# Kernel tuning notes

Measured on AMD Instinct MI355X. Metric: run time of the kernel, lower is better.

The kernel has to match this reference:

```python
import jax, jax.numpy as jnp
import numpy as np

N_Q, N_X, N_Z = 512, 256, 256
N = N_Q + N_X + N_Z  # 1024 nodes per graph
H = 128
B = 128
EPS = 1e-5


def _bn(x, g, b):
    # BatchNorm1d in training mode: biased stats over all but last axis
    ax = tuple(range(x.ndim - 1))
    m = x.mean(ax)
    v = x.var(ax)
    return (x - m) * jax.lax.rsqrt(v + EPS) * g + b


def _node_feats():
    # buffer 'single_nodes': one-hot [qubit, x-check, z-check]
    f = jnp.zeros((N, 3), jnp.float32)
    f = f.at[:N_Q, 0].set(1.0)
    f = f.at[N_Q:N_Q + N_X, 1].set(1.0)
    f = f.at[N_Q + N_X:, 2].set(1.0)
    return f


def setup_inputs() -> dict:
    key = jax.random.key(0)
    ks = jax.random.split(key, 16)

    def lin(k, i, o):
        return (jax.random.normal(k, (i, o), jnp.float32) / np.sqrt(i)).astype(jnp.float32)

    return {
        "adj": jax.random.randint(ks[0], (B, N, N), 0, 2, dtype=jnp.int32),
        "w0a": lin(ks[1], 3, H), "b0a": jnp.zeros((H,), jnp.float32),
        "w0b": lin(ks[2], H, H), "b0b": jnp.zeros((H,), jnp.float32),
        "w1a": lin(ks[3], H, H), "b1a": jnp.zeros((H,), jnp.float32),
        "w1b": lin(ks[4], H, H), "b1b": jnp.zeros((H,), jnp.float32),
        "w2a": lin(ks[5], H, H), "b2a": jnp.zeros((H,), jnp.float32),
        "w2b": lin(ks[6], H, H), "b2b": jnp.zeros((H,), jnp.float32),
        "bn_in_g": jnp.ones((3,), jnp.float32), "bn_in_b": jnp.zeros((3,), jnp.float32),
        "bn0_g": jnp.ones((H,), jnp.float32), "bn0_b": jnp.zeros((H,), jnp.float32),
        "bn1_g": jnp.ones((H,), jnp.float32), "bn1_b": jnp.zeros((H,), jnp.float32),
        "bn2_g": jnp.ones((H,), jnp.float32), "bn2_b": jnp.zeros((H,), jnp.float32),
        "ln_g": jnp.ones((H,), jnp.float32), "ln_b": jnp.zeros((H,), jnp.float32),
        "fc1_w": lin(ks[7], H, 256), "fc1_b": jnp.zeros((256,), jnp.float32),
        "fcbn1_g": jnp.ones((256,), jnp.float32), "fcbn1_b": jnp.zeros((256,), jnp.float32),
        "fc2_w": lin(ks[8], 256, 512), "fc2_b": jnp.zeros((512,), jnp.float32),
        "fcbn2_g": jnp.ones((512,), jnp.float32), "fcbn2_b": jnp.zeros((512,), jnp.float32),
        "fc3_w": lin(ks[9], 512, 1), "fc3_b": jnp.zeros((1,), jnp.float32),
    }


def reference(adj, w0a, b0a, w0b, b0b, w1a, b1a, w1b, b1b, w2a, b2a, w2b, b2b,
              bn_in_g, bn_in_b, bn0_g, bn0_b, bn1_g, bn1_b, bn2_g, bn2_b,
              ln_g, ln_b, fc1_w, fc1_b, fcbn1_g, fcbn1_b, fc2_w, fc2_b,
              fcbn2_g, fcbn2_b, fc3_w, fc3_b):
    leaky = lambda z: jax.nn.leaky_relu(z, 0.1)
    Af = adj.astype(jnp.float32)                       # [B,N,N]
    x = jnp.broadcast_to(_node_feats(), (adj.shape[0], N, 3))
    x = _bn(x, bn_in_g, bn_in_b)                       # input BatchNorm1d(3)
    h = x

    mlps = [(w0a, b0a, w0b, b0b, jax.nn.relu, bn0_g, bn0_b),
            (w1a, b1a, w1b, b1b, leaky, bn1_g, bn1_b),
            (w2a, b2a, w2b, b2b, leaky, bn2_g, bn2_b)]
    for i, (wa, ba, wb, bb, act, g, b) in enumerate(mlps):
        # GINConv (eps=0): aggregate = h_i + sum_{j: edge j->i} h_j = h + A^T h
        agg = h + jnp.einsum('bji,bjd->bid', Af, h)
        m = act(agg @ wa + ba) @ wb + bb               # GIN MLP
        m = _bn(m, g, b)
        h = jax.nn.relu(m + (h if i > 0 else 0.0))

    pooled = h.mean(axis=1)                            # global_mean_pool -> [B,H]
    mu = pooled.mean(-1, keepdims=True)
    var = pooled.var(-1, keepdims=True)
    out = (pooled - mu) * jax.lax.rsqrt(var + EPS) * ln_g + ln_b  # LayerNorm

    z = leaky(_bn(out @ fc1_w + fc1_b, fcbn1_g, fcbn1_b))
    z = leaky(_bn(z @ fc2_w + fc2_b, fcbn2_g, fcbn2_b))
    return z @ fc3_w + fc3_b                           # [B,1]
```

## Files before the change

### kernel.cpp

```cpp
#include <hip/hip_runtime.h>
#include <hip/hip_bf16.h>

typedef float f32x4 __attribute__((ext_vector_type(4)));
typedef _Float16 half8 __attribute__((ext_vector_type(8)));
typedef _Float16 half4 __attribute__((ext_vector_type(4)));

__device__ __forceinline__ unsigned short f2h(float f) {
  return __builtin_bit_cast(unsigned short, (_Float16)f);
}
__device__ __forceinline__ float h2f(unsigned short u) {
  return (float)__builtin_bit_cast(_Float16, u);
}
__device__ __forceinline__ unsigned expand2(unsigned b2) {
  return (b2 & 1u) * 0x3C00u + ((b2 >> 1) & 1u) * 0x3C000000u;
}
__device__ __forceinline__ half8 expand8(unsigned v) {
  uint4 u;
  u.x = expand2(v);
  u.y = expand2(v >> 2);
  u.z = expand2(v >> 4);
  u.w = expand2(v >> 6);
  return __builtin_bit_cast(half8, u);
}

__global__ __launch_bounds__(256) void k_pack(const int* __restrict__ adj,
    unsigned* __restrict__ Abits, float* __restrict__ cnt,
    const float* __restrict__ w0b, const float* __restrict__ w1a,
    const float* __restrict__ w1b, const float* __restrict__ w2a,
    const float* __restrict__ w2b, unsigned short* __restrict__ wT) {
  __shared__ int tile[64 * 129];
  __shared__ unsigned bitT[128 * 33];
  __shared__ float cred[256 * 3];
  int blk = blockIdx.x;
  if (blk >= 1024) {
    int wb = blk - 1024;
    if (threadIdx.x < 128) {
      int mat = wb >> 7, k = wb & 127, dd = threadIdx.x;
      const float* src = (mat == 0) ? w0b : (mat == 1) ? w1a : (mat == 2) ? w1b
                        : (mat == 3) ? w2a : w2b;
      wT[mat * 16384 + dd * 128 + k] = f2h(src[k * 128 + dd]);
    }
    return;
  }
  int b = blk >> 3, i0 = (blk & 7) << 7;
  int t = threadIdx.x;
  int il = t & 127, js = t >> 7;
  int c0 = 0, c1 = 0, c2 = 0;
  for (int jt = 0; jt < 16; ++jt) {
    int jbase = jt << 6;
    __syncthreads();
    for (int p = 0; p < 8; ++p) {
      int f = p * 256 + t;
      int row = f >> 5, i4 = (f & 31) << 2;
      *reinterpret_cast<int4*>(&tile[row * 129 + i4]) =
        *reinterpret_cast<const int4*>(&adj[((size_t)b << 20) + ((size_t)(jbase + row) << 10) + i0 + i4]);
    }
    __syncthreads();
    unsigned wbits = 0;
    int csum = 0;
    for (int r = 0; r < 32; ++r) {
      int jl = js * 32 + r;
      int a = tile[jl * 129 + il] & 1;
      csum += a;
      wbits |= (unsigned)a << r;
    }
    bitT[il * 33 + jt * 2 + js] = wbits;
    if (jt < 8) c0 += csum; else if (jt < 12) c1 += csum; else c2 += csum;
  }
  cred[t * 3 + 0] = (float)c0;
  cred[t * 3 + 1] = (float)c1;
  cred[t * 3 + 2] = (float)c2;
  __syncthreads();
  if (t < 128) {
    for (int c = 0; c < 3; ++c)
      cnt[(((size_t)b << 10) + i0 + t) * 4 + c] = cred[t * 3 + c] + cred[(t + 128) * 3 + c];
  }
  unsigned* dst = Abits + ((size_t)b << 15) + ((size_t)i0 << 5);
  for (int q = 0; q < 16; ++q) {
    int f = t + 256 * q;
    dst[f] = bitT[(f >> 5) * 33 + (f & 31)];
  }
}

__global__ __launch_bounds__(256) void k_layer(const unsigned* __restrict__ Abits,
    const unsigned short* __restrict__ h_t,
    const unsigned short* __restrict__ waT, const float* __restrict__ ba,
    const unsigned short* __restrict__ wbT, const float* __restrict__ bb,
    unsigned short* __restrict__ m_out, float* __restrict__ ps, float* __restrict__ pq) {
  __shared__ __align__(16) unsigned short smem[18432];
  unsigned short* tb0 = smem;
  unsigned short* tb1 = smem + 9216;
  unsigned short* tz = smem;
  int d = blockIdx.x;
  int b = (d & 7) + ((d >> 6) << 3);
  int i0 = ((d >> 3) & 7) << 7;
  int t = threadIdx.x;
  int w = t >> 6, lane = t & 63;
  int wr = (w >> 1) * 64, wc = (w & 1) * 64;
  int lr = lane & 15, lk8 = (lane >> 4) * 8;
  const unsigned* Ab = Abits + ((size_t)b << 15);

  f32x4 acc[4][4] = {};
  {
    for (int q = 0; q < 4; ++q) {
      int c = t * 4 + q;
      int r = c >> 3, off = (c & 7) << 3;
      *reinterpret_cast<uint4*>(&tb0[r * 72 + off]) =
        *reinterpret_cast<const uint4*>(&h_t[(((size_t)b << 7) + r) * 1024 + off]);
    }
  }
  __syncthreads();
  for (int jt = 0; jt < 16; ++jt) {
    unsigned short* cur = (jt & 1) ? tb1 : tb0;
    unsigned short* nxt = (jt & 1) ? tb0 : tb1;
    if (jt < 15) {
      for (int q = 0; q < 4; ++q) {
        int c = t * 4 + q;
        int r = c >> 3, off = (c & 7) << 3;
        *reinterpret_cast<uint4*>(&nxt[r * 72 + off]) =
          *reinterpret_cast<const uint4*>(&h_t[(((size_t)b << 7) + r) * 1024 + ((jt + 1) << 6) + off]);
      }
    }
    uint2 w01[4];
#pragma unroll
    for (int x = 0; x < 4; ++x)
      w01[x] = *reinterpret_cast<const uint2*>(&Ab[(i0 + wr + x * 16 + lr) * 32 + jt * 2]);
#pragma unroll
    for (int ks = 0; ks < 2; ++ks) {
      half8 bfr[4];
#pragma unroll
      for (int x = 0; x < 4; ++x)
        bfr[x] = *reinterpret_cast<const half8*>(&cur[(wc + x * 16 + lr) * 72 + ks * 32 + lk8]);
      half8 af[4];
#pragma unroll
      for (int x = 0; x < 4; ++x) {
        unsigned wk = ks ? w01[x].y : w01[x].x;
        af[x] = expand8(wk >> lk8);
      }
#pragma unroll
      for (int x = 0; x < 4; ++x)
#pragma unroll
        for (int y = 0; y < 4; ++y)
          acc[x][y] = __builtin_amdgcn_mfma_f32_16x16x32_f16(af[x], bfr[y], acc[x][y], 0, 0, 0);
    }
    __syncthreads();
  }
  for (int x = 0; x < 4; ++x)
    for (int y = 0; y < 4; ++y) {
      int col = wc + y * 16 + lr;
      int row0 = wr + x * 16 + ((lane >> 4) << 2);
      uint2 rbits = *reinterpret_cast<const uint2*>(
          &h_t[((size_t)(b * 128 + col)) * 1024 + i0 + row0]);
      half4 rh = __builtin_bit_cast(half4, rbits);
      for (int q = 0; q < 4; ++q)
        tz[(row0 + q) * 136 + col] = f2h(acc[x][y][q] + (float)rh[q]);
    }
  __syncthreads();
  f32x4 acc2[4][4] = {};
#pragma unroll
  for (int kt = 0; kt < 2; ++kt)
#pragma unroll
    for (int ks = 0; ks < 2; ++ks) {
      int k0 = kt * 64 + ks * 32 + lk8;
      half8 af[4], bw[4];
#pragma unroll
      for (int x = 0; x < 4; ++x)
        af[x] = *reinterpret_cast<const half8*>(&tz[(wr + x * 16 + lr) * 136 + k0]);
#pragma unroll
      for (int x = 0; x < 4; ++x)
        bw[x] = *reinterpret_cast<const half8*>(&waT[(wc + x * 16 + lr) * 128 + k0]);
#pragma unroll
      for (int x = 0; x < 4; ++x)
#pragma unroll
        for (int y = 0; y < 4; ++y)
          acc2[x][y] = __builtin_amdgcn_mfma_f32_16x16x32_f16(af[x], bw[y], acc2[x][y], 0, 0, 0);
    }
  __syncthreads();
  for (int x = 0; x < 4; ++x)
    for (int y = 0; y < 4; ++y)
      for (int q = 0; q < 4; ++q) {
        int row = wr + x * 16 + ((lane >> 4) << 2) + q;
        int col = wc + y * 16 + lr;
        float vv = acc2[x][y][q] + ba[col];
        vv = vv > 0.f ? vv : 0.1f * vv;
        tz[row * 136 + col] = f2h(vv);
      }
  __syncthreads();
  f32x4 acc3[4][4] = {};
#pragma unroll
  for (int kt = 0; kt < 2; ++kt)
#pragma unroll
    for (int ks = 0; ks < 2; ++ks) {
      int k0 = kt * 64 + ks * 32 + lk8;
      half8 af[4], bw[4];
#pragma unroll
      for (int x = 0; x < 4; ++x)
        af[x] = *reinterpret_cast<const half8*>(&tz[(wr + x * 16 + lr) * 136 + k0]);
#pragma unroll
      for (int x = 0; x < 4; ++x)
        bw[x] = *reinterpret_cast<const half8*>(&wbT[(wc + x * 16 + lr) * 128 + k0]);
#pragma unroll
      for (int x = 0; x < 4; ++x)
#pragma unroll
        for (int y = 0; y < 4; ++y)
          acc3[x][y] = __builtin_amdgcn_mfma_f32_16x16x32_f16(af[x], bw[y], acc3[x][y], 0, 0, 0);
    }
  float s[4] = {}, q2[4] = {};
  for (int x = 0; x < 4; ++x)
    for (int y = 0; y < 4; ++y)
      for (int q = 0; q < 4; ++q) {
        int row = wr + x * 16 + ((lane >> 4) << 2) + q;
        int col = wc + y * 16 + lr;
        float vv = acc3[x][y][q] + bb[col];
        m_out[(((size_t)b << 10) + i0 + row) * 128 + col] = f2h(vv);
        s[y] += vv; q2[y] += vv * vv;
      }
  __syncthreads();
  float* fs = (float*)smem;
  float* fq = fs + 1024;
  int slot = (w >> 1) * 4 + (lane >> 4);
  for (int y = 0; y < 4; ++y) {
    int col = wc + y * 16 + lr;
    fs[col * 8 + slot] = s[y];
    fq[col * 8 + slot] = q2[y];
  }
  __syncthreads();
  if (t < 128) {
    float S = 0, Q = 0;
    for (int k = 0; k < 8; ++k) { S += fs[t * 8 + k]; Q += fq[t * 8 + k]; }
    ps[d * 128 + t] = S;
    pq[d * 128 + t] = Q;
  }
}

__global__ __launch_bounds__(256) void k_layer0(const float* __restrict__ cnt,
    const float* __restrict__ w0a, const float* __restrict__ b0a,
    const float* __restrict__ g3, const float* __restrict__ bb3,
    const unsigned short* __restrict__ wbT, const float* __restrict__ bb,
    unsigned short* __restrict__ m_out, float* __restrict__ ps, float* __restrict__ pq) {
  __shared__ __align__(16) unsigned short smem[17408];
  unsigned short* tz = smem;
  int blk = blockIdx.x;
  int b = blk >> 3, i0 = (blk & 7) << 7;
  int t = threadIdx.x;
  int w = t >> 6, lane = t & 63;
  int wr = (w >> 1) * 64, wc = (w & 1) * 64;
  int lr = lane & 15, lk8 = (lane >> 4) * 8;

  const float mean3[3] = {0.5f, 0.25f, 0.25f};
  const float var3[3] = {0.25f, 0.1875f, 0.1875f};
  float v[3][3];
  for (int c = 0; c < 3; ++c) {
    float rs = rsqrtf(var3[c] + 1e-5f) * g3[c];
    for (int tt = 0; tt < 3; ++tt)
      v[tt][c] = ((tt == c ? 1.f : 0.f) - mean3[c]) * rs + bb3[c];
  }
  int rr = t >> 1, hf = t & 1;
  int i = i0 + rr;
  int ty = i < 512 ? 0 : (i < 768 ? 1 : 2);
  const float* cc = cnt + (((size_t)b << 10) + i) * 4;
  float a0 = v[ty][0] + cc[0] * v[0][0] + cc[1] * v[1][0] + cc[2] * v[2][0];
  float a1 = v[ty][1] + cc[0] * v[0][1] + cc[1] * v[1][1] + cc[2] * v[2][1];
  float a2 = v[ty][2] + cc[0] * v[0][2] + cc[1] * v[1][2] + cc[2] * v[2][2];
  for (int c = 0; c < 64; ++c) {
    int col = hf * 64 + c;
    float z = a0 * w0a[col] + a1 * w0a[128 + col] + a2 * w0a[256 + col] + b0a[col];
    tz[rr * 136 + col] = f2h(fmaxf(z, 0.f));
  }
  __syncthreads();
  f32x4 acc3[4][4] = {};
#pragma unroll
  for (int kt = 0; kt < 2; ++kt)
#pragma unroll
    for (int ks = 0; ks < 2; ++ks) {
      int k0 = kt * 64 + ks * 32 + lk8;
      half8 af[4], bw[4];
#pragma unroll
      for (int x = 0; x < 4; ++x)
        af[x] = *reinterpret_cast<const half8*>(&tz[(wr + x * 16 + lr) * 136 + k0]);
#pragma unroll
      for (int x = 0; x < 4; ++x)
        bw[x] = *reinterpret_cast<const half8*>(&wbT[(wc + x * 16 + lr) * 128 + k0]);
#pragma unroll
      for (int x = 0; x < 4; ++x)
#pragma unroll
        for (int y = 0; y < 4; ++y)
          acc3[x][y] = __builtin_amdgcn_mfma_f32_16x16x32_f16(af[x], bw[y], acc3[x][y], 0, 0, 0);
    }
  float s[4] = {}, q2[4] = {};
  for (int x = 0; x < 4; ++x)
    for (int y = 0; y < 4; ++y)
      for (int q = 0; q < 4; ++q) {
        int row = wr + x * 16 + ((lane >> 4) << 2) + q;
        int col = wc + y * 16 + lr;
        float vv = acc3[x][y][q] + bb[col];
        m_out[(((size_t)b << 10) + i0 + row) * 128 + col] = f2h(vv);
        s[y] += vv; q2[y] += vv * vv;
      }
  __syncthreads();
  float* fs = (float*)smem;
  float* fq = fs + 1024;
  int slot = (w >> 1) * 4 + (lane >> 4);
  for (int y = 0; y < 4; ++y) {
    int col = wc + y * 16 + lr;
    fs[col * 8 + slot] = s[y];
    fq[col * 8 + slot] = q2[y];
  }
  __syncthreads();
  if (t < 128) {
    float S = 0, Q = 0;
    for (int k = 0; k < 8; ++k) { S += fs[t * 8 + k]; Q += fq[t * 8 + k]; }
    ps[blk * 128 + t] = S;
    pq[blk * 128 + t] = Q;
  }
}

__global__ __launch_bounds__(256) void k_bnred(const float* __restrict__ ps,
    const float* __restrict__ pq, const float* __restrict__ g,
    const float* __restrict__ be, float* __restrict__ st) {
  __shared__ float rs[4], rq[4];
  int ch = blockIdx.x, t = threadIdx.x;
  float s = 0, q = 0;
  for (int k = t; k < 1024; k += 256) {
    s += ps[k * 128 + ch]; q += pq[k * 128 + ch];
  }
  for (int off = 32; off; off >>= 1) {
    s += __shfl_down(s, off); q += __shfl_down(q, off);
  }
  if ((t & 63) == 0) { rs[t >> 6] = s; rq[t >> 6] = q; }
  __syncthreads();
  if (t == 0) {
    s = rs[0] + rs[1] + rs[2] + rs[3];
    q = rq[0] + rq[1] + rq[2] + rq[3];
    float mean = s * (1.f / 131072.f);
    float var = q * (1.f / 131072.f) - mean * mean;
    float sc = g[ch] * rsqrtf(var + 1e-5f);
    st[ch * 2] = sc;
    st[ch * 2 + 1] = be[ch] - mean * sc;
  }
}

__global__ __launch_bounds__(256) void k_apply(const unsigned short* __restrict__ m,
    const float* __restrict__ st, unsigned short* __restrict__ h_rm,
    unsigned short* __restrict__ h_t, float* __restrict__ pool_ps,
    int use_res, int write_t, int do_pool) {
  __shared__ unsigned short lt[128 * 130];
  __shared__ float lp[128 * 16];
  int blk = blockIdx.x;
  int b = blk >> 3, i0 = (blk & 7) << 7;
  int t = threadIdx.x;
  int chg = t & 15, rowg = t >> 4;
  int ch0 = chg * 8;
  float sc[8], sh[8];
#pragma unroll
  for (int j = 0; j < 8; ++j) { sc[j] = st[(ch0 + j) * 2]; sh[j] = st[(ch0 + j) * 2 + 1]; }
  float psum[8] = {};
  for (int it = 0; it < 8; ++it) {
    int row = it * 16 + rowg;
    size_t base = ((((size_t)b << 10) + i0 + row) << 7) + ch0;
    half8 mv = *reinterpret_cast<const half8*>(&m[base]);
    half8 rv{};
    if (use_res) rv = *reinterpret_cast<const half8*>(&h_rm[base]);
    half8 out;
#pragma unroll
    for (int j = 0; j < 8; ++j) {
      float vv = (float)mv[j] * sc[j] + sh[j];
      if (use_res) vv += (float)rv[j];
      vv = fmaxf(vv, 0.f);
      _Float16 hv = (_Float16)vv;
      out[j] = hv;
      psum[j] += (float)hv;
      lt[(ch0 + j) * 130 + row] = __builtin_bit_cast(unsigned short, hv);
    }
    *reinterpret_cast<half8*>(&h_rm[base]) = out;
  }
  if (write_t) {
    __syncthreads();
    for (int it = 0; it < 32; ++it) {
      int ch2 = it * 4 + (t >> 6);
      int p = (t & 63) * 2;
      unsigned u0 = lt[ch2 * 130 + p];
      unsigned u1 = lt[ch2 * 130 + p + 1];
      *reinterpret_cast<unsigned*>(&h_t[(((size_t)b << 7) + ch2) * 1024 + i0 + p]) = u0 | (u1 << 16);
    }
  }
  if (do_pool) {
#pragma unroll
    for (int j = 0; j < 8; ++j) lp[(ch0 + j) * 16 + rowg] = psum[j];
    __syncthreads();
    if (t < 128) {
      float S = 0;
      for (int k = 0; k < 16; ++k) S += lp[t * 16 + k];
      pool_ps[blk * 128 + t] = S;
    }
  }
}

__global__ __launch_bounds__(256) void k_poolfc1(const float* __restrict__ pool_ps,
    const float* __restrict__ ln_g, const float* __restrict__ ln_b,
    const float* __restrict__ w, const float* __restrict__ bias,
    float* __restrict__ y1) {
  __shared__ float ln[128];
  __shared__ float stat[2];
  int b = blockIdx.x, t = threadIdx.x;
  if (t < 128) {
    float s = 0;
    for (int k = 0; k < 8; ++k) s += pool_ps[((b << 3) + k) * 128 + t];
    ln[t] = s * (1.f / 1024.f);
  }
  __syncthreads();
  if (t < 64) {
    float a = ln[t], c = ln[t + 64];
    float ss = a + c, qq = a * a + c * c;
    for (int off = 32; off; off >>= 1) { ss += __shfl_down(ss, off); qq += __shfl_down(qq, off); }
    if (t == 0) {
      float mean = ss * (1.f / 128.f);
      float var = qq * (1.f / 128.f) - mean * mean;
      stat[0] = mean; stat[1] = rsqrtf(var + 1e-5f);
    }
  }
  __syncthreads();
  if (t < 128) ln[t] = (ln[t] - stat[0]) * stat[1] * ln_g[t] + ln_b[t];
  __syncthreads();
  float s = bias[t];
  for (int k = 0; k < 128; ++k) s += ln[k] * w[k * 256 + t];
  y1[b * 256 + t] = s;
}

__global__ void k_fc2(const float* __restrict__ z1, const float* __restrict__ w,
                      const float* __restrict__ bias, float* __restrict__ y) {
  int b = blockIdx.x, c = threadIdx.x;
  const float* x = z1 + b * 256;
  float s = bias[c];
  for (int k = 0; k < 256; ++k) s += x[k] * w[k * 512 + c];
  y[b * 512 + c] = s;
}
__global__ void k_bnhead(const float* __restrict__ y, float* __restrict__ z,
                         const float* __restrict__ g, const float* __restrict__ be, int C) {
  int c = threadIdx.x;
  float s = 0, q = 0;
  for (int b = 0; b < 128; ++b) { float v = y[b * C + c]; s += v; q += v * v; }
  float mean = s * (1.f / 128.f);
  float var = q * (1.f / 128.f) - mean * mean;
  float sc = g[c] * rsqrtf(var + 1e-5f);
  float sh = be[c] - mean * sc;
  for (int b = 0; b < 128; ++b) {
    float v = y[b * C + c] * sc + sh;
    z[b * C + c] = v > 0.f ? v : 0.1f * v;
  }
}
__global__ void k_fc3(const float* __restrict__ z2, const float* __restrict__ w,
                      const float* __restrict__ bias, float* __restrict__ out) {
  int b = blockIdx.x, t = threadIdx.x;
  float s = 0;
  for (int k = t; k < 512; k += 64) s += z2[b * 512 + k] * w[k];
  for (int off = 32; off; off >>= 1) s += __shfl_down(s, off);
  if (t == 0) out[b] = s + bias[0];
}

extern "C" void kernel_launch(void* const* d_in, const int* in_sizes, int n_in,
                              void* d_out, int out_size, void* d_ws, size_t ws_size,
                              hipStream_t stream) {
  const int* adj = (const int*)d_in[0];
  const float* w0a = (const float*)d_in[1];
  const float* b0a = (const float*)d_in[2];
  const float* b0b = (const float*)d_in[4];
  const float* b1a = (const float*)d_in[6];
  const float* b1b = (const float*)d_in[8];
  const float* b2a = (const float*)d_in[10];
  const float* b2b = (const float*)d_in[12];
  const float* bn_in_g = (const float*)d_in[13];
  const float* bn_in_b = (const float*)d_in[14];
  const float* bn0_g = (const float*)d_in[15];
  const float* bn0_b = (const float*)d_in[16];
  const float* bn1_g = (const float*)d_in[17];
  const float* bn1_b = (const float*)d_in[18];
  const float* bn2_g = (const float*)d_in[19];
  const float* bn2_b = (const float*)d_in[20];
  const float* ln_g = (const float*)d_in[21];
  const float* ln_b = (const float*)d_in[22];
  const float* fc1_w = (const float*)d_in[23];
  const float* fc1_b = (const float*)d_in[24];
  const float* fcbn1_g = (const float*)d_in[25];
  const float* fcbn1_b = (const float*)d_in[26];
  const float* fc2_w = (const float*)d_in[27];
  const float* fc2_b = (const float*)d_in[28];
  const float* fcbn2_g = (const float*)d_in[29];
  const float* fcbn2_b = (const float*)d_in[30];
  const float* fc3_w = (const float*)d_in[31];
  const float* fc3_b = (const float*)d_in[32];

  char* ws = (char*)d_ws;
  size_t need = 122127360;
  if (ws_size < need) return;

  unsigned* Abits = (unsigned*)ws;
  size_t off = 16777216;
  float* cnt = (float*)(ws + off); off += 2097152;
  unsigned short* h_rm = (unsigned short*)(ws + off); off += 33554432;
  unsigned short* h_t  = (unsigned short*)(ws + off); off += 33554432;
  unsigned short* mbuf = (unsigned short*)(ws + off); off += 33554432;
  unsigned short* wT = (unsigned short*)(ws + off); off += 163840;
  float* ps = (float*)(ws + off); off += 524288;
  float* pq = (float*)(ws + off); off += 524288;
  float* pool_ps = (float*)(ws + off); off += 524288;
  float* st = (float*)(ws + off); off += 1024;
  float* y1 = (float*)(ws + off); off += 131072;
  float* z1 = (float*)(ws + off); off += 131072;
  float* y2 = (float*)(ws + off); off += 262144;
  float* z2 = (float*)(ws + off); off += 262144;

  float* out = (float*)d_out;

  k_pack<<<dim3(1664), dim3(256), 0, stream>>>(adj, Abits, cnt,
      (const float*)d_in[3], (const float*)d_in[5], (const float*)d_in[7],
      (const float*)d_in[9], (const float*)d_in[11], wT);
  k_layer0<<<dim3(1024), dim3(256), 0, stream>>>(cnt, w0a, b0a, bn_in_g, bn_in_b,
      wT + 0 * 16384, b0b, mbuf, ps, pq);
  k_bnred<<<dim3(128), dim3(256), 0, stream>>>(ps, pq, bn0_g, bn0_b, st);
  k_apply<<<dim3(1024), dim3(256), 0, stream>>>(mbuf, st, h_rm, h_t, pool_ps, 0, 1, 0);
  k_layer<<<dim3(1024), dim3(256), 0, stream>>>(Abits, h_t,
      wT + 1 * 16384, b1a, wT + 2 * 16384, b1b, mbuf, ps, pq);
  k_bnred<<<dim3(128), dim3(256), 0, stream>>>(ps, pq, bn1_g, bn1_b, st);
  k_apply<<<dim3(1024), dim3(256), 0, stream>>>(mbuf, st, h_rm, h_t, pool_ps, 1, 1, 0);
  k_layer<<<dim3(1024), dim3(256), 0, stream>>>(Abits, h_t,
      wT + 3 * 16384, b2a, wT + 4 * 16384, b2b, mbuf, ps, pq);
  k_bnred<<<dim3(128), dim3(256), 0, stream>>>(ps, pq, bn2_g, bn2_b, st);
  k_apply<<<dim3(1024), dim3(256), 0, stream>>>(mbuf, st, h_rm, h_t, pool_ps, 1, 0, 1);
  k_poolfc1<<<dim3(128), dim3(256), 0, stream>>>(pool_ps, ln_g, ln_b, fc1_w, fc1_b, y1);
  k_bnhead<<<dim3(1), dim3(256), 0, stream>>>(y1, z1, fcbn1_g, fcbn1_b, 256);
  k_fc2<<<dim3(128), dim3(512), 0, stream>>>(z1, fc2_w, fc2_b, y2);
  k_bnhead<<<dim3(1), dim3(512), 0, stream>>>(y2, z2, fcbn2_g, fcbn2_b, 512);
  k_fc3<<<dim3(128), dim3(64), 0, stream>>>(z2, fc3_w, fc3_b, out);
}
```

Baseline: 432.7 us.

## Rework adjacency packing, widen h_t stores, skip unused writes, fuse head kernels

The adjacency pack kernel now reads int4 rows straight from global memory into per-thread bit words instead of staging a tile in LDS, and computes the per-type counts with popcount over the packed bits. k_apply pads its LDS transpose to stride 131, writes the transposed output with 8-byte stores, and skips the row-major h store on the last layer where nothing reads it. The MLP head merges BatchNorm with the following FC layer (each block recomputes the batch statistics redundantly), which removes two single-block kernels and their intermediate buffers. The expand2 bit trick is simplified to a single multiply.

```diff
diff --git a/kernel.cpp b/kernel.cpp
--- a/kernel.cpp
+++ b/kernel.cpp
@@ -12,7 +12,7 @@
   return (float)__builtin_bit_cast(_Float16, u);
 }
 __device__ __forceinline__ unsigned expand2(unsigned b2) {
-  return (b2 & 1u) * 0x3C00u + ((b2 >> 1) & 1u) * 0x3C000000u;
+  return ((b2 & 1u) | ((b2 & 2u) << 15)) * 0x3C00u;
 }
 __device__ __forceinline__ half8 expand8(unsigned v) {
   uint4 u;
@@ -28,7 +28,6 @@
     const float* __restrict__ w0b, const float* __restrict__ w1a,
     const float* __restrict__ w1b, const float* __restrict__ w2a,
     const float* __restrict__ w2b, unsigned short* __restrict__ wT) {
-  __shared__ int tile[64 * 129];
   __shared__ unsigned bitT[128 * 33];
   __shared__ float cred[256 * 3];
   int blk = blockIdx.x;
@@ -44,32 +43,42 @@
   }
   int b = blk >> 3, i0 = (blk & 7) << 7;
   int t = threadIdx.x;
-  int il = t & 127, js = t >> 7;
-  int c0 = 0, c1 = 0, c2 = 0;
-  for (int jt = 0; jt < 16; ++jt) {
+  int g = t >> 6;
+  int u = t & 63, iq = u & 31, js = u >> 5;
+  for (int o = 0; o < 4; ++o) {
+    int jt = o * 4 + g;
     int jbase = jt << 6;
-    __syncthreads();
-    for (int p = 0; p < 8; ++p) {
-      int f = p * 256 + t;
-      int row = f >> 5, i4 = (f & 31) << 2;
-      *reinterpret_cast<int4*>(&tile[row * 129 + i4]) =
-        *reinterpret_cast<const int4*>(&adj[((size_t)b << 20) + ((size_t)(jbase + row) << 10) + i0 + i4]);
-    }
-    __syncthreads();
-    unsigned wbits = 0;
-    int csum = 0;
+    unsigned b0 = 0, b1 = 0, b2 = 0, b3 = 0;
     for (int r = 0; r < 32; ++r) {
       int jl = js * 32 + r;
-      int a = tile[jl * 129 + il] & 1;
-      csum += a;
-      wbits |= (unsigned)a << r;
-    }
-    bitT[il * 33 + jt * 2 + js] = wbits;
-    if (jt < 8) c0 += csum; else if (jt < 12) c1 += csum; else c2 += csum;
-  }
-  cred[t * 3 + 0] = (float)c0;
-  cred[t * 3 + 1] = (float)c1;
-  cred[t * 3 + 2] = (float)c2;
+      int4 v = *reinterpret_cast<const int4*>(
+          &adj[((size_t)b << 20) + ((size_t)(jbase + jl) << 10) + i0 + iq * 4]);
+      b0 |= (unsigned)(v.x & 1) << r;
+      b1 |= (unsigned)(v.y & 1) << r;
+      b2 |= (unsigned)(v.z & 1) << r;
+      b3 |= (unsigned)(v.w & 1) << r;
+    }
+    int base = (iq * 4) * 33 + jt * 2 + js;
+    bitT[base] = b0;
+    bitT[base + 33] = b1;
+    bitT[base + 66] = b2;
+    bitT[base + 99] = b3;
+  }
+  __syncthreads();
+  {
+    int il = t & 127, half = t >> 7;
+    float c0 = 0, c1 = 0, c2 = 0;
+    for (int mi = 0; mi < 16; ++mi) {
+      int m = half * 16 + mi;
+      int pc = __popc(bitT[il * 33 + m]);
+      if (half == 0) c0 += pc;
+      else if (m < 24) c1 += pc;
+      else c2 += pc;
+    }
+    cred[t * 3 + 0] = c0;
+    cred[t * 3 + 1] = c1;
+    cred[t * 3 + 2] = c2;
+  }
   __syncthreads();
   if (t < 128) {
     for (int c = 0; c < 3; ++c)
@@ -344,7 +353,7 @@
     const float* __restrict__ st, unsigned short* __restrict__ h_rm,
     unsigned short* __restrict__ h_t, float* __restrict__ pool_ps,
     int use_res, int write_t, int do_pool) {
-  __shared__ unsigned short lt[128 * 130];
+  __shared__ unsigned short lt[128 * 131];
   __shared__ float lp[128 * 16];
   int blk = blockIdx.x;
   int b = blk >> 3, i0 = (blk & 7) << 7;
@@ -370,18 +379,22 @@
       _Float16 hv = (_Float16)vv;
       out[j] = hv;
       psum[j] += (float)hv;
-      lt[(ch0 + j) * 130 + row] = __builtin_bit_cast(unsigned short, hv);
-    }
-    *reinterpret_cast<half8*>(&h_rm[base]) = out;
+      lt[(ch0 + j) * 131 + row] = __builtin_bit_cast(unsigned short, hv);
+    }
+    if (write_t)
+      *reinterpret_cast<half8*>(&h_rm[base]) = out;
   }
   if (write_t) {
     __syncthreads();
-    for (int it = 0; it < 32; ++it) {
-      int ch2 = it * 4 + (t >> 6);
-      int p = (t & 63) * 2;
-      unsigned u0 = lt[ch2 * 130 + p];
-      unsigned u1 = lt[ch2 * 130 + p + 1];
-      *reinterpret_cast<unsigned*>(&h_t[(((size_t)b << 7) + ch2) * 1024 + i0 + p]) = u0 | (u1 << 16);
+    for (int it = 0; it < 16; ++it) {
+      int ch2 = it * 8 + (t >> 5);
+      int pu = (t & 31) * 4;
+      unsigned u0 = lt[ch2 * 131 + pu];
+      unsigned u1 = lt[ch2 * 131 + pu + 1];
+      unsigned u2 = lt[ch2 * 131 + pu + 2];
+      unsigned u3 = lt[ch2 * 131 + pu + 3];
+      uint2 vv; vv.x = u0 | (u1 << 16); vv.y = u2 | (u3 << 16);
+      *reinterpret_cast<uint2*>(&h_t[(((size_t)b << 7) + ch2) * 1024 + i0 + pu]) = vv;
     }
   }
   if (do_pool) {
@@ -427,35 +440,53 @@
   y1[b * 256 + t] = s;
 }
 
-__global__ void k_fc2(const float* __restrict__ z1, const float* __restrict__ w,
-                      const float* __restrict__ bias, float* __restrict__ y) {
-  int b = blockIdx.x, c = threadIdx.x;
-  const float* x = z1 + b * 256;
-  float s = bias[c];
-  for (int k = 0; k < 256; ++k) s += x[k] * w[k * 512 + c];
-  y[b * 512 + c] = s;
-}
-__global__ void k_bnhead(const float* __restrict__ y, float* __restrict__ z,
-                         const float* __restrict__ g, const float* __restrict__ be, int C) {
-  int c = threadIdx.x;
+__global__ __launch_bounds__(512) void k_fc2bn(const float* __restrict__ y1,
+    const float* __restrict__ g, const float* __restrict__ be,
+    const float* __restrict__ w, const float* __restrict__ bias,
+    float* __restrict__ y2) {
+  __shared__ float z1s[256];
+  int b = blockIdx.x, t = threadIdx.x;
+  if (t < 256) {
+    float s = 0, q = 0;
+    for (int bb = 0; bb < 128; ++bb) { float v = y1[bb * 256 + t]; s += v; q += v * v; }
+    float mean = s * (1.f / 128.f);
+    float var = q * (1.f / 128.f) - mean * mean;
+    float sc = g[t] * rsqrtf(var + 1e-5f);
+    float sh = be[t] - mean * sc;
+    float v = y1[b * 256 + t] * sc + sh;
+    z1s[t] = v > 0.f ? v : 0.1f * v;
+  }
+  __syncthreads();
+  float s = bias[t];
+  for (int k = 0; k < 256; ++k) s += z1s[k] * w[k * 512 + t];
+  y2[b * 512 + t] = s;
+}
+
+__global__ __launch_bounds__(512) void k_fc3bn(const float* __restrict__ y2,
+    const float* __restrict__ g, const float* __restrict__ be,
+    const float* __restrict__ w, const float* __restrict__ bias,
+    float* __restrict__ out) {
+  __shared__ float red[512];
+  int b = blockIdx.x, t = threadIdx.x;
   float s = 0, q = 0;
-  for (int b = 0; b < 128; ++b) { float v = y[b * C + c]; s += v; q += v * v; }
+  for (int bb = 0; bb < 128; ++bb) { float v = y2[bb * 512 + t]; s += v; q += v * v; }
   float mean = s * (1.f / 128.f);
   float var = q * (1.f / 128.f) - mean * mean;
-  float sc = g[c] * rsqrtf(var + 1e-5f);
-  float sh = be[c] - mean * sc;
-  for (int b = 0; b < 128; ++b) {
-    float v = y[b * C + c] * sc + sh;
-    z[b * C + c] = v > 0.f ? v : 0.1f * v;
-  }
-}
-__global__ void k_fc3(const float* __restrict__ z2, const float* __restrict__ w,
-                      const float* __restrict__ bias, float* __restrict__ out) {
-  int b = blockIdx.x, t = threadIdx.x;
-  float s = 0;
-  for (int k = t; k < 512; k += 64) s += z2[b * 512 + k] * w[k];
-  for (int off = 32; off; off >>= 1) s += __shfl_down(s, off);
-  if (t == 0) out[b] = s + bias[0];
+  float sc = g[t] * rsqrtf(var + 1e-5f);
+  float sh = be[t] - mean * sc;
+  float v = y2[b * 512 + t] * sc + sh;
+  v = v > 0.f ? v : 0.1f * v;
+  red[t] = v * w[t];
+  __syncthreads();
+  if (t < 256) red[t] += red[t + 256];
+  __syncthreads();
+  if (t < 128) red[t] += red[t + 128];
+  __syncthreads();
+  if (t < 64) {
+    float x = red[t] + red[t + 64];
+    for (int off = 32; off; off >>= 1) x += __shfl_down(x, off);
+    if (t == 0) out[b] = x + bias[0];
+  }
 }
 
 extern "C" void kernel_launch(void* const* d_in, const int* in_sizes, int n_in,
@@ -506,9 +537,7 @@
   float* pool_ps = (float*)(ws + off); off += 524288;
   float* st = (float*)(ws + off); off += 1024;
   float* y1 = (float*)(ws + off); off += 131072;
-  float* z1 = (float*)(ws + off); off += 131072;
   float* y2 = (float*)(ws + off); off += 262144;
-  float* z2 = (float*)(ws + off); off += 262144;
 
   float* out = (float*)d_out;
 
@@ -528,8 +557,6 @@
   k_bnred<<<dim3(128), dim3(256), 0, stream>>>(ps, pq, bn2_g, bn2_b, st);
   k_apply<<<dim3(1024), dim3(256), 0, stream>>>(mbuf, st, h_rm, h_t, pool_ps, 1, 0, 1);
   k_poolfc1<<<dim3(128), dim3(256), 0, stream>>>(pool_ps, ln_g, ln_b, fc1_w, fc1_b, y1);
-  k_bnhead<<<dim3(1), dim3(256), 0, stream>>>(y1, z1, fcbn1_g, fcbn1_b, 256);
-  k_fc2<<<dim3(128), dim3(512), 0, stream>>>(z1, fc2_w, fc2_b, y2);
-  k_bnhead<<<dim3(1), dim3(512), 0, stream>>>(y2, z2, fcbn2_g, fcbn2_b, 512);
-  k_fc3<<<dim3(128), dim3(64), 0, stream>>>(z2, fc3_w, fc3_b, out);
-}
+  k_fc2bn<<<dim3(128), dim3(512), 0, stream>>>(y1, fcbn1_g, fcbn1_b, fc2_w, fc2_b, y2);
+  k_fc3bn<<<dim3(128), dim3(512), 0, stream>>>(y2, fcbn2_g, fcbn2_b, fc3_w, fc3_b, out);
+}
```

New measurement: 411.1 us, median of 2. 1.05x faster.
